# Optimization experiments

Measured on AMD Instinct MI355X. Metric: run time of the kernel, lower is better.

Reference implementation:

```python
import jax, jax.numpy as jnp
import numpy as np

N = 100000          # nodes
E = 1600000         # edges
F = 128             # input features
H = 128             # hidden_channels
G = 64              # graphs in batch


def setup_inputs() -> dict:
    key = jax.random.key(0)
    ks = jax.random.split(key, 16)
    x = jax.random.normal(ks[0], (N, F), dtype=jnp.float32)
    edge_index = jax.random.randint(ks[1], (2, E), 0, N, dtype=jnp.int32)
    batch = jnp.sort(jax.random.randint(ks[2], (N,), 0, G, dtype=jnp.int32))

    def glorot(k, fan_in, fan_out):
        s = jnp.sqrt(6.0 / (fan_in + fan_out)).astype(jnp.float32)
        return jax.random.uniform(k, (fan_in, fan_out), jnp.float32, -s, s)

    return {
        "x": x, "edge_index": edge_index, "batch": batch,
        "W1": glorot(ks[3], F, H),       "b1": jnp.zeros((H,), jnp.float32),
        "W2": glorot(ks[4], H, H),       "b2": jnp.zeros((H,), jnp.float32),
        "W3": glorot(ks[5], H, 2 * H),   "b3": jnp.zeros((2 * H,), jnp.float32),
        "W4": glorot(ks[6], 2 * H, H),   "b4": jnp.zeros((H,), jnp.float32),
        "Wl": glorot(ks[7], F, H),       "bl": jnp.zeros((H,), jnp.float32),
    }


def _gcn_conv(x, W, b, src, dst, deg_inv_sqrt):
    # PyG GCNConv: add self-loops, symmetric normalization D^-1/2 (A+I) D^-1/2
    h = x @ W                                  # [N, out]
    norm = deg_inv_sqrt[src] * deg_inv_sqrt[dst]      # [E]
    msg = h[src] * norm[:, None]               # gather + scale, [E, out]
    agg = jax.ops.segment_sum(msg, dst, num_segments=N)
    agg = agg + h * (deg_inv_sqrt * deg_inv_sqrt)[:, None]  # self-loop term (norm = 1/deg)
    return agg + b


def reference(x, edge_index, batch, W1, b1, W2, b2, W3, b3, W4, b4, Wl, bl):
    src, dst = edge_index[0], edge_index[1]
    # degree (incl. self-loop) from dst, as in PyG gcn_norm
    deg = jax.ops.segment_sum(jnp.ones((E,), jnp.float32), dst, num_segments=N) + 1.0
    deg_inv_sqrt = jax.lax.rsqrt(deg)

    identity = x
    x = jax.nn.relu(_gcn_conv(x, W1, b1, src, dst, deg_inv_sqrt))
    x = jax.nn.relu(_gcn_conv(x, W2, b2, src, dst, deg_inv_sqrt))
    x = jax.nn.relu(_gcn_conv(x, W3, b3, src, dst, deg_inv_sqrt))
    x = _gcn_conv(x, W4, b4, src, dst, deg_inv_sqrt)
    x = x + (identity @ Wl + bl)

    # global_mean_pool over graph ids
    sums = jax.ops.segment_sum(x, batch, num_segments=G)
    cnts = jax.ops.segment_sum(jnp.ones((N,), jnp.float32), batch, num_segments=G)
    return sums / jnp.maximum(cnts, 1.0)[:, None]
```

## Files before the change

kernel.cpp:

```cpp
#include <hip/hip_runtime.h>

#define NN 100000
#define EE 1600000
#define GG 64
#define PCHUNK 1024
#define PBLK 1563
#define NBUCK 196

typedef __attribute__((ext_vector_type(8))) short short8v;
typedef __attribute__((ext_vector_type(4))) float f32x4;

__device__ __forceinline__ unsigned short f2bf(float f) {
    unsigned u = __float_as_uint(f);
    u = (u + 0x7FFFu + ((u >> 16) & 1)) >> 16;
    return (unsigned short)u;
}
__device__ __forceinline__ float bf2f(unsigned short s) {
    return __uint_as_float((unsigned)s << 16);
}

__global__ __launch_bounds__(256) void partitionA_kernel(const int* __restrict__ src,
                                                         const int* __restrict__ dst,
                                                         int* __restrict__ cnt,
                                                         int* __restrict__ ghist,
                                                         int* __restrict__ gboff,
                                                         int2* __restrict__ stage) {
    __shared__ int hist[NBUCK];
    __shared__ int sc[256];
    __shared__ int boff[NBUCK];
    __shared__ int bcur[NBUCK];
    int b = blockIdx.x, t = threadIdx.x;
    int e0 = b * PCHUNK;
    int n = EE - e0;
    if (n > PCHUNK) n = PCHUNK;
    if (t < NBUCK) { hist[t] = 0; bcur[t] = 0; }
    __syncthreads();
    int dv[4], sv[4];
#pragma unroll
    for (int j = 0; j < 4; ++j) {
        int i = t + j * 256;
        if (i < n) {
            dv[j] = dst[e0 + i];
            sv[j] = src[e0 + i];
            atomicAdd(&cnt[dv[j]], 1);
            atomicAdd(&hist[dv[j] >> 9], 1);
        }
    }
    __syncthreads();
    sc[t] = (t < NBUCK) ? hist[t] : 0;
    __syncthreads();
    for (int off = 1; off < 256; off <<= 1) {
        int a = (t >= off) ? sc[t - off] : 0;
        __syncthreads();
        sc[t] += a;
        __syncthreads();
    }
    if (t < NBUCK) boff[t] = sc[t] - hist[t];
    __syncthreads();
#pragma unroll
    for (int j = 0; j < 4; ++j) {
        int i = t + j * 256;
        if (i < n) {
            int k = dv[j] >> 9;
            int p = boff[k] + atomicAdd(&bcur[k], 1);
            stage[(size_t)b * PCHUNK + p] = make_int2(sv[j], dv[j]);
        }
    }
    if (t < NBUCK) {
        ghist[b * NBUCK + t] = hist[t];
        gboff[b * NBUCK + t] = boff[t];
    }
}

__global__ __launch_bounds__(256) void dis_kernel(const int* __restrict__ cnt,
                                                  float* __restrict__ dis) {
    int i = blockIdx.x * 256 + threadIdx.x;
    if (i < NN) dis[i] = rsqrtf((float)cnt[i] + 1.0f);
}

#define SCAN_EPB 1024
__global__ __launch_bounds__(256) void scan_block_kernel(const int* __restrict__ in,
                                                         int* __restrict__ out,
                                                         int* __restrict__ bsums) {
    __shared__ int sd[256];
    int t = threadIdx.x;
    int base = blockIdx.x * SCAN_EPB + t * 4;
    int v[4];
#pragma unroll
    for (int j = 0; j < 4; ++j) v[j] = (base + j < NN) ? in[base + j] : 0;
    int s = v[0] + v[1] + v[2] + v[3];
    sd[t] = s;
    __syncthreads();
    for (int off = 1; off < 256; off <<= 1) {
        int add = (t >= off) ? sd[t - off] : 0;
        __syncthreads();
        sd[t] += add;
        __syncthreads();
    }
    int ex = sd[t] - s;
    int run = ex;
#pragma unroll
    for (int j = 0; j < 4; ++j) {
        if (base + j < NN) out[base + j] = run;
        run += v[j];
    }
    if (t == 255) bsums[blockIdx.x] = sd[255];
}

__global__ void scan_sums_kernel(int* __restrict__ bsums, int nb) {
    if (threadIdx.x == 0 && blockIdx.x == 0) {
        int run = 0;
        for (int i = 0; i < nb; ++i) {
            int v = bsums[i];
            bsums[i] = run;
            run += v;
        }
    }
}

__global__ __launch_bounds__(256) void scan_add_kernel(int* __restrict__ rs,
                                                       const int* __restrict__ bsums,
                                                       int* __restrict__ cursor) {
    int i = blockIdx.x * 256 + threadIdx.x;
    if (i < NN) {
        int v = rs[i] + bsums[i >> 10];
        rs[i] = v;
        cursor[i] = v;
    }
    if (i == 0) rs[NN] = EE;
}

__global__ __launch_bounds__(256) void scatterC_kernel(const int2* __restrict__ stage,
                                                       const int* __restrict__ ghist,
                                                       const int* __restrict__ gboff,
                                                       int* __restrict__ cursor,
                                                       int* __restrict__ csr) {
    int k = blockIdx.x;
    int b = blockIdx.y * 256 + threadIdx.x;
    if (b >= PBLK) return;
    int c_ = ghist[b * NBUCK + k];
    size_t base = (size_t)b * PCHUNK + gboff[b * NBUCK + k];
    for (int i = 0; i < c_; ++i) {
        int2 e = stage[base + i];
        int p = atomicAdd(&cursor[e.y], 1);
        csr[p] = e.x;
    }
}

__global__ __launch_bounds__(256) void cvt_kernel(const float* __restrict__ x,
                                                  const float* __restrict__ dis,
                                                  unsigned short* __restrict__ xb) {
    size_t i = ((size_t)blockIdx.x * 256 + threadIdx.x) * 8;
    float d = dis[i >> 7];
    float4 a = *(const float4*)(x + i);
    float4 b = *(const float4*)(x + i + 4);
    short8v v;
    v[0] = (short)f2bf(a.x * d); v[1] = (short)f2bf(a.y * d);
    v[2] = (short)f2bf(a.z * d); v[3] = (short)f2bf(a.w * d);
    v[4] = (short)f2bf(b.x * d); v[5] = (short)f2bf(b.y * d);
    v[6] = (short)f2bf(b.z * d); v[7] = (short)f2bf(b.w * d);
    *(short8v*)(xb + i) = v;
}

template <int K, int M>
__global__ __launch_bounds__(64) void packw_kernel(const float* __restrict__ W,
                                                   unsigned short* __restrict__ Wp) {
    const int NKS = K / 32;
    int ct = blockIdx.x / NKS, ks = blockIdx.x % NKS;
    int lane = threadIdx.x;
    int col = ct * 16 + (lane & 15);
    int kb = ks * 32 + (lane >> 4) * 8;
    unsigned short* o = Wp + ((size_t)(ct * NKS + ks) * 64 + lane) * 16;
#pragma unroll
    for (int i = 0; i < 8; ++i) {
        float f = W[(size_t)(kb + i) * M + col];
        unsigned short h = f2bf(f);
        unsigned short l = f2bf(f - bf2f(h));
        o[i] = h;
        o[8 + i] = l;
    }
}

template <int K, int M, int RT, bool ASPLIT, bool RELU, bool BIAS, bool ACCUM, bool DSCALE>
__global__ __launch_bounds__(256) void gemm_kernel(const void* __restrict__ Ain,
                                                   const unsigned short* __restrict__ Wp,
                                                   const float* __restrict__ bias,
                                                   const float* __restrict__ dis,
                                                   void* __restrict__ out) {
    const int NKS = K / 32;
    int tid = threadIdx.x;
    int wave = tid >> 6, lane = tid & 63;
    int r0 = blockIdx.x * (RT * 64) + wave * (RT * 16);

    short8v ah[RT][NKS];
    short8v al[ASPLIT ? RT : 1][ASPLIT ? NKS : 1];
#pragma unroll
    for (int t = 0; t < RT; ++t) {
        int ra = r0 + t * 16 + (lane & 15);
        if (ra > NN - 1) ra = NN - 1;
        if (ASPLIT) {
            const float* A = (const float*)Ain;
#pragma unroll
            for (int ks = 0; ks < NKS; ++ks) {
                const float* p = A + (size_t)ra * K + ks * 32 + (lane >> 4) * 8;
                float4 v0 = *(const float4*)p;
                float4 v1 = *(const float4*)(p + 4);
                float f[8] = {v0.x, v0.y, v0.z, v0.w, v1.x, v1.y, v1.z, v1.w};
#pragma unroll
                for (int i = 0; i < 8; ++i) {
                    unsigned short h = f2bf(f[i]);
                    ah[t][ks][i] = (short)h;
                    al[t][ks][i] = (short)f2bf(f[i] - bf2f(h));
                }
            }
        } else {
            const unsigned short* A = (const unsigned short*)Ain;
#pragma unroll
            for (int ks = 0; ks < NKS; ++ks)
                ah[t][ks] = *(const short8v*)(A + (size_t)ra * K + ks * 32 + (lane >> 4) * 8);
        }
    }

    float dsc[RT][4];
#pragma unroll
    for (int t = 0; t < RT; ++t)
#pragma unroll
        for (int i = 0; i < 4; ++i) {
            int row = r0 + t * 16 + (lane >> 4) * 4 + i;
            dsc[t][i] = (DSCALE && row < NN) ? dis[row] : 1.f;
        }

#pragma unroll
    for (int ct = 0; ct < 8; ++ct) {
        int ctg = blockIdx.y * 8 + ct;
        int col = ctg * 16 + (lane & 15);
        float bv = BIAS ? bias[col] : 0.f;
        f32x4 acc[RT];
#pragma unroll
        for (int t = 0; t < RT; ++t) {
            acc[t][0] = bv; acc[t][1] = bv; acc[t][2] = bv; acc[t][3] = bv;
        }
#pragma unroll
        for (int ks = 0; ks < NKS; ++ks) {
            const short8v* pW = (const short8v*)Wp + ((size_t)(ctg * NKS + ks) * 64 + lane) * 2;
            short8v bh = pW[0], blo = pW[1];
#pragma unroll
            for (int t = 0; t < RT; ++t) {
                acc[t] = __builtin_amdgcn_mfma_f32_16x16x32_bf16(ah[t][ks], bh, acc[t], 0, 0, 0);
                acc[t] = __builtin_amdgcn_mfma_f32_16x16x32_bf16(ah[t][ks], blo, acc[t], 0, 0, 0);
                if (ASPLIT)
                    acc[t] = __builtin_amdgcn_mfma_f32_16x16x32_bf16(al[t][ks], bh, acc[t], 0, 0, 0);
            }
        }
#pragma unroll
        for (int t = 0; t < RT; ++t)
#pragma unroll
            for (int i = 0; i < 4; ++i) {
                int row = r0 + t * 16 + (lane >> 4) * 4 + i;
                if (row >= NN) continue;
                float v = acc[t][i];
                if (RELU) v = fmaxf(v, 0.f);
                if (ACCUM) {
                    ((float*)out)[(size_t)row * M + col] += v;
                } else {
                    ((unsigned short*)out)[(size_t)row * M + col] = f2bf(v * dsc[t][i]);
                }
            }
    }
}

template <int OUTMODE>
__global__ __launch_bounds__(256) void aggb_kernel(const unsigned short* __restrict__ h,
                                                   const float* __restrict__ dis,
                                                   const int* __restrict__ csr,
                                                   const int* __restrict__ rs,
                                                   const float* __restrict__ bias,
                                                   void* __restrict__ out) {
    int node = blockIdx.x * 4 + (threadIdx.x >> 6);
    int lane = threadIdx.x & 63;
    if (node >= NN) return;
    int c = lane & 15;
    int s = lane >> 4;
    int beg = rs[node], end = rs[node + 1];
    const uint4* hb = (const uint4*)h;
    float acc[8] = {};
    for (int e0 = beg; e0 < end; e0 += 32) {
        int myidx = 0;
        int el = e0 + lane;
        if (lane < 32 && el < end) myidx = csr[el];
        uint4 v[8];
#pragma unroll
        for (int j = 0; j < 8; ++j) {
            int sidx = __shfl(myidx, j * 4 + s, 64);
            v[j] = make_uint4(0u, 0u, 0u, 0u);
            int ej = e0 + j * 4 + s;
            if (ej < end) v[j] = hb[(size_t)sidx * 16 + c];
        }
#pragma unroll
        for (int j = 0; j < 8; ++j) {
            acc[0] += __uint_as_float(v[j].x << 16);
            acc[1] += __uint_as_float(v[j].x & 0xFFFF0000u);
            acc[2] += __uint_as_float(v[j].y << 16);
            acc[3] += __uint_as_float(v[j].y & 0xFFFF0000u);
            acc[4] += __uint_as_float(v[j].z << 16);
            acc[5] += __uint_as_float(v[j].z & 0xFFFF0000u);
            acc[6] += __uint_as_float(v[j].w << 16);
            acc[7] += __uint_as_float(v[j].w & 0xFFFF0000u);
        }
    }
#pragma unroll
    for (int i = 0; i < 8; ++i) {
        acc[i] += __shfl_xor(acc[i], 16, 64);
        acc[i] += __shfl_xor(acc[i], 32, 64);
    }
    if (s == 0) {
        float d = dis[node];
        uint4 us = hb[(size_t)node * 16 + c];
        float sf[8];
        sf[0] = __uint_as_float(us.x << 16); sf[1] = __uint_as_float(us.x & 0xFFFF0000u);
        sf[2] = __uint_as_float(us.y << 16); sf[3] = __uint_as_float(us.y & 0xFFFF0000u);
        sf[4] = __uint_as_float(us.z << 16); sf[5] = __uint_as_float(us.z & 0xFFFF0000u);
        sf[6] = __uint_as_float(us.w << 16); sf[7] = __uint_as_float(us.w & 0xFFFF0000u);
        float r[8];
#pragma unroll
        for (int i = 0; i < 8; ++i) r[i] = d * (acc[i] + sf[i]);
        if (OUTMODE == 0) {
            uint4 o;
            o.x = (unsigned)f2bf(r[0]) | ((unsigned)f2bf(r[1]) << 16);
            o.y = (unsigned)f2bf(r[2]) | ((unsigned)f2bf(r[3]) << 16);
            o.z = (unsigned)f2bf(r[4]) | ((unsigned)f2bf(r[5]) << 16);
            o.w = (unsigned)f2bf(r[6]) | ((unsigned)f2bf(r[7]) << 16);
            ((uint4*)out)[(size_t)node * 16 + c] = o;
        } else {
#pragma unroll
            for (int i = 0; i < 8; ++i) r[i] += bias[c * 8 + i];
            float4 o0 = make_float4(r[0], r[1], r[2], r[3]);
            float4 o1 = make_float4(r[4], r[5], r[6], r[7]);
            float* O = (float*)out + (size_t)node * 128 + c * 8;
            *(float4*)O = o0;
            *(float4*)(O + 4) = o1;
        }
    }
}

__global__ __launch_bounds__(128) void pool_partial_kernel(const float* __restrict__ y,
                                                           const int* __restrict__ batch,
                                                           float* __restrict__ P) {
    int c = threadIdx.x;
    int chunk = (NN + gridDim.x - 1) / gridDim.x;
    int n0 = blockIdx.x * chunk;
    int n1 = n0 + chunk;
    if (n1 > NN) n1 = NN;
    if (n0 >= NN) return;
    int curg = batch[n0];
    float acc = 0.f;
    for (int n = n0; n < n1; ++n) {
        int g = batch[n];
        if (g != curg) {
            atomicAdd(&P[curg * 128 + c], acc);
            acc = 0.f;
            curg = g;
        }
        acc += y[(size_t)n * 128 + c];
    }
    atomicAdd(&P[curg * 128 + c], acc);
}

__global__ __launch_bounds__(128) void pool_final_kernel(const float* __restrict__ P,
                                                         const int* __restrict__ batch,
                                                         float* __restrict__ out) {
    int g = blockIdx.x, c = threadIdx.x;
    int lo = 0, hi = NN;
    while (lo < hi) {
        int m = (lo + hi) >> 1;
        if (batch[m] < g) lo = m + 1;
        else hi = m;
    }
    int start = lo;
    int lo2 = start, hi2 = NN;
    while (lo2 < hi2) {
        int m = (lo2 + hi2) >> 1;
        if (batch[m] < g + 1) lo2 = m + 1;
        else hi2 = m;
    }
    float cntg = (float)(lo2 - start);
    out[g * 128 + c] = P[g * 128 + c] / fmaxf(cntg, 1.f);
}

extern "C" void kernel_launch(void* const* d_in, const int* in_sizes, int n_in,
                              void* d_out, int out_size, void* d_ws, size_t ws_size,
                              hipStream_t stream) {
    const float* x = (const float*)d_in[0];
    const int* ei = (const int*)d_in[1];
    const int* batch = (const int*)d_in[2];
    const float* W1 = (const float*)d_in[3];
    const float* b1 = (const float*)d_in[4];
    const float* W2 = (const float*)d_in[5];
    const float* b2 = (const float*)d_in[6];
    const float* W3 = (const float*)d_in[7];
    const float* b3 = (const float*)d_in[8];
    const float* W4 = (const float*)d_in[9];
    const float* b4 = (const float*)d_in[10];
    const float* Wl = (const float*)d_in[11];
    const float* bl = (const float*)d_in[12];
    float* out = (float*)d_out;

    char* p = (char*)d_ws;
    auto alloc = [&](size_t bytes) {
        void* r = (void*)p;
        p += (bytes + 255) & ~(size_t)255;
        return r;
    };
    int* cnt = (int*)alloc((size_t)NN * 4);
    int* rs = (int*)alloc((size_t)(NN + 1) * 4);
    int* cursor = (int*)alloc((size_t)NN * 4);
    float* dis = (float*)alloc((size_t)NN * 4);
    const int NB = (NN + SCAN_EPB - 1) / SCAN_EPB;
    int* bsums = (int*)alloc((size_t)NB * 4);
    int* csr = (int*)alloc((size_t)EE * 4);
    int* ghist = (int*)alloc((size_t)PBLK * NBUCK * 4);
    int* gboff = (int*)alloc((size_t)PBLK * NBUCK * 4);
    unsigned short* xb = (unsigned short*)alloc((size_t)NN * 128 * 2);
    unsigned short* AG = (unsigned short*)alloc((size_t)NN * 128 * 2);
    unsigned short* GM = (unsigned short*)alloc((size_t)NN * 128 * 2);
    unsigned short* H3 = (unsigned short*)alloc((size_t)NN * 256 * 2);
    float* Y = (float*)alloc((size_t)NN * 128 * 4);
    unsigned short* W1p = (unsigned short*)alloc(8 * 4 * 64 * 16 * 2);
    unsigned short* W2p = (unsigned short*)alloc(8 * 4 * 64 * 16 * 2);
    unsigned short* W3p = (unsigned short*)alloc(16 * 4 * 64 * 16 * 2);
    unsigned short* W4p = (unsigned short*)alloc(8 * 8 * 64 * 16 * 2);
    unsigned short* Wlp = (unsigned short*)alloc(8 * 4 * 64 * 16 * 2);
    float* P = (float*)alloc((size_t)GG * 128 * 4);
    int2* stage = (int2*)Y;

    const int* src = ei;
    const int* dst = ei + EE;

    hipMemsetAsync(cnt, 0, (size_t)NN * 4, stream);
    hipMemsetAsync(P, 0, (size_t)GG * 128 * 4, stream);

    partitionA_kernel<<<PBLK, 256, 0, stream>>>(src, dst, cnt, ghist, gboff, stage);
    dis_kernel<<<(NN + 255) / 256, 256, 0, stream>>>(cnt, dis);
    cvt_kernel<<<(NN * 128) / (256 * 8), 256, 0, stream>>>(x, dis, xb);
    scan_block_kernel<<<NB, 256, 0, stream>>>(cnt, rs, bsums);
    scan_sums_kernel<<<1, 64, 0, stream>>>(bsums, NB);
    scan_add_kernel<<<(NN + 255) / 256, 256, 0, stream>>>(rs, bsums, cursor);
    scatterC_kernel<<<dim3(NBUCK, (PBLK + 255) / 256), 256, 0, stream>>>(stage, ghist, gboff, cursor, csr);

    packw_kernel<128, 128><<<8 * 4, 64, 0, stream>>>(W1, W1p);
    packw_kernel<128, 128><<<8 * 4, 64, 0, stream>>>(W2, W2p);
    packw_kernel<128, 256><<<16 * 4, 64, 0, stream>>>(W3, W3p);
    packw_kernel<256, 128><<<8 * 8, 64, 0, stream>>>(W4, W4p);
    packw_kernel<128, 128><<<8 * 4, 64, 0, stream>>>(Wl, Wlp);

    const int AGG_GRID = (NN + 3) / 4;
    const int GX4 = (NN + 255) / 256;
    const int GX2 = (NN + 127) / 128;

    aggb_kernel<0><<<AGG_GRID, 256, 0, stream>>>(xb, dis, csr, rs, nullptr, AG);
    gemm_kernel<128, 128, 4, false, true, true, false, true><<<dim3(GX4, 1), 256, 0, stream>>>(AG, W1p, b1, dis, GM);
    aggb_kernel<0><<<AGG_GRID, 256, 0, stream>>>(GM, dis, csr, rs, nullptr, AG);
    gemm_kernel<128, 128, 4, false, true, true, false, true><<<dim3(GX4, 1), 256, 0, stream>>>(AG, W2p, b2, dis, GM);
    aggb_kernel<0><<<AGG_GRID, 256, 0, stream>>>(GM, dis, csr, rs, nullptr, AG);
    gemm_kernel<128, 256, 4, false, true, true, false, false><<<dim3(GX4, 2), 256, 0, stream>>>(AG, W3p, b3, nullptr, H3);
    gemm_kernel<256, 128, 2, false, false, false, false, true><<<dim3(GX2, 1), 256, 0, stream>>>(H3, W4p, nullptr, dis, AG);
    aggb_kernel<1><<<AGG_GRID, 256, 0, stream>>>(AG, dis, csr, rs, b4, Y);
    gemm_kernel<128, 128, 2, true, false, true, true, false><<<dim3(GX2, 1), 256, 0, stream>>>(x, Wlp, bl, nullptr, Y);
    pool_partial_kernel<<<512, 128, 0, stream>>>(Y, batch, P);
    pool_final_kernel<<<GG, 128, 0, stream>>>(P, batch, out);
}
```

Baseline: 798.4 us.

## Replace multi-pass CSR build with two-pass bucket sort and per-bucket local CSR

Rebuilds the CSR construction as a two-level bucket sort. A first kernel atomically reserves slots per 512-node bucket in fixed-capacity staging regions. A single-block scan then computes bucket bases, and a per-bucket kernel builds node histograms, row starts, degree normalisation and CSR entries entirely in shared memory. This drops the global per-node count atomics, the multi-kernel scan and the scatter kernel that used global cursor atomics. The trade-off is a fixed per-bucket capacity (BWCAP) that silently drops edges if a bucket overflows, which only holds for evenly spread destinations. CSR order within a node also becomes nondeterministic.

```diff
diff --git a/kernel.cpp b/kernel.cpp
--- a/kernel.cpp
+++ b/kernel.cpp
@@ -3,9 +3,10 @@
 #define NN 100000
 #define EE 1600000
 #define GG 64
-#define PCHUNK 1024
-#define PBLK 1563
+#define PCHUNK 2048
+#define PBLK1 782
 #define NBUCK 196
+#define BWCAP 12288
 
 typedef __attribute__((ext_vector_type(8))) short short8v;
 typedef __attribute__((ext_vector_type(4))) float f32x4;
@@ -19,35 +20,50 @@
     return __uint_as_float((unsigned)s << 16);
 }
 
-__global__ __launch_bounds__(256) void partitionA_kernel(const int* __restrict__ src,
-                                                         const int* __restrict__ dst,
-                                                         int* __restrict__ cnt,
-                                                         int* __restrict__ ghist,
-                                                         int* __restrict__ gboff,
-                                                         int2* __restrict__ stage) {
+__global__ __launch_bounds__(256) void bucketK1_kernel(const int* __restrict__ src,
+                                                       const int* __restrict__ dst,
+                                                       int* __restrict__ gcur,
+                                                       int2* __restrict__ stage) {
     __shared__ int hist[NBUCK];
-    __shared__ int sc[256];
-    __shared__ int boff[NBUCK];
-    __shared__ int bcur[NBUCK];
+    __shared__ int base[NBUCK];
+    __shared__ int cur[NBUCK];
     int b = blockIdx.x, t = threadIdx.x;
     int e0 = b * PCHUNK;
     int n = EE - e0;
     if (n > PCHUNK) n = PCHUNK;
-    if (t < NBUCK) { hist[t] = 0; bcur[t] = 0; }
-    __syncthreads();
-    int dv[4], sv[4];
-#pragma unroll
-    for (int j = 0; j < 4; ++j) {
+    if (t < NBUCK) { hist[t] = 0; cur[t] = 0; }
+    __syncthreads();
+    int dv[8], sv[8];
+#pragma unroll
+    for (int j = 0; j < 8; ++j) {
         int i = t + j * 256;
         if (i < n) {
             dv[j] = dst[e0 + i];
             sv[j] = src[e0 + i];
-            atomicAdd(&cnt[dv[j]], 1);
             atomicAdd(&hist[dv[j] >> 9], 1);
         }
     }
     __syncthreads();
-    sc[t] = (t < NBUCK) ? hist[t] : 0;
+    if (t < NBUCK && hist[t] > 0) base[t] = atomicAdd(&gcur[t], hist[t]);
+    __syncthreads();
+#pragma unroll
+    for (int j = 0; j < 8; ++j) {
+        int i = t + j * 256;
+        if (i < n) {
+            int k = dv[j] >> 9;
+            int p = base[k] + atomicAdd(&cur[k], 1);
+            if (p < BWCAP) stage[(size_t)k * BWCAP + p] = make_int2(sv[j], dv[j]);
+        }
+    }
+}
+
+__global__ __launch_bounds__(256) void kscan_kernel(const int* __restrict__ gcur,
+                                                    int* __restrict__ bbase,
+                                                    int* __restrict__ rs) {
+    __shared__ int sc[256];
+    int t = threadIdx.x;
+    int v = (t < NBUCK) ? gcur[t] : 0;
+    sc[t] = v;
     __syncthreads();
     for (int off = 1; off < 256; off <<= 1) {
         int a = (t >= off) ? sc[t - off] : 0;
@@ -55,95 +71,58 @@
         sc[t] += a;
         __syncthreads();
     }
-    if (t < NBUCK) boff[t] = sc[t] - hist[t];
-    __syncthreads();
-#pragma unroll
-    for (int j = 0; j < 4; ++j) {
-        int i = t + j * 256;
-        if (i < n) {
-            int k = dv[j] >> 9;
-            int p = boff[k] + atomicAdd(&bcur[k], 1);
-            stage[(size_t)b * PCHUNK + p] = make_int2(sv[j], dv[j]);
-        }
-    }
-    if (t < NBUCK) {
-        ghist[b * NBUCK + t] = hist[t];
-        gboff[b * NBUCK + t] = boff[t];
-    }
-}
-
-__global__ __launch_bounds__(256) void dis_kernel(const int* __restrict__ cnt,
-                                                  float* __restrict__ dis) {
-    int i = blockIdx.x * 256 + threadIdx.x;
-    if (i < NN) dis[i] = rsqrtf((float)cnt[i] + 1.0f);
-}
-
-#define SCAN_EPB 1024
-__global__ __launch_bounds__(256) void scan_block_kernel(const int* __restrict__ in,
-                                                         int* __restrict__ out,
-                                                         int* __restrict__ bsums) {
-    __shared__ int sd[256];
-    int t = threadIdx.x;
-    int base = blockIdx.x * SCAN_EPB + t * 4;
-    int v[4];
-#pragma unroll
-    for (int j = 0; j < 4; ++j) v[j] = (base + j < NN) ? in[base + j] : 0;
-    int s = v[0] + v[1] + v[2] + v[3];
-    sd[t] = s;
+    if (t < NBUCK) bbase[t] = sc[t] - v;
+    if (t == 0) rs[NN] = EE;
+}
+
+__global__ __launch_bounds__(256) void buildK2_kernel(const int2* __restrict__ stage,
+                                                      const int* __restrict__ gcur,
+                                                      const int* __restrict__ bbase,
+                                                      float* __restrict__ dis,
+                                                      int* __restrict__ rs,
+                                                      int* __restrict__ csr) {
+    __shared__ int hist[512];
+    __shared__ int lrs[512];
+    __shared__ int cur[512];
+    __shared__ int sc[256];
+    int k = blockIdx.x, t = threadIdx.x;
+    int cnt_ = gcur[k];
+    if (cnt_ > BWCAP) cnt_ = BWCAP;
+    const int2* W = stage + (size_t)k * BWCAP;
+    hist[t] = 0; hist[t + 256] = 0;
+    cur[t] = 0; cur[t + 256] = 0;
+    __syncthreads();
+    for (int i = t; i < cnt_; i += 256) atomicAdd(&hist[W[i].y & 511], 1);
+    __syncthreads();
+    int h0 = hist[2 * t], h1 = hist[2 * t + 1];
+    sc[t] = h0 + h1;
     __syncthreads();
     for (int off = 1; off < 256; off <<= 1) {
-        int add = (t >= off) ? sd[t - off] : 0;
+        int a = (t >= off) ? sc[t - off] : 0;
         __syncthreads();
-        sd[t] += add;
+        sc[t] += a;
         __syncthreads();
     }
-    int ex = sd[t] - s;
-    int run = ex;
-#pragma unroll
-    for (int j = 0; j < 4; ++j) {
-        if (base + j < NN) out[base + j] = run;
-        run += v[j];
-    }
-    if (t == 255) bsums[blockIdx.x] = sd[255];
-}
-
-__global__ void scan_sums_kernel(int* __restrict__ bsums, int nb) {
-    if (threadIdx.x == 0 && blockIdx.x == 0) {
-        int run = 0;
-        for (int i = 0; i < nb; ++i) {
-            int v = bsums[i];
-            bsums[i] = run;
-            run += v;
-        }
-    }
-}
-
-__global__ __launch_bounds__(256) void scan_add_kernel(int* __restrict__ rs,
-                                                       const int* __restrict__ bsums,
-                                                       int* __restrict__ cursor) {
-    int i = blockIdx.x * 256 + threadIdx.x;
-    if (i < NN) {
-        int v = rs[i] + bsums[i >> 10];
-        rs[i] = v;
-        cursor[i] = v;
-    }
-    if (i == 0) rs[NN] = EE;
-}
-
-__global__ __launch_bounds__(256) void scatterC_kernel(const int2* __restrict__ stage,
-                                                       const int* __restrict__ ghist,
-                                                       const int* __restrict__ gboff,
-                                                       int* __restrict__ cursor,
-                                                       int* __restrict__ csr) {
-    int k = blockIdx.x;
-    int b = blockIdx.y * 256 + threadIdx.x;
-    if (b >= PBLK) return;
-    int c_ = ghist[b * NBUCK + k];
-    size_t base = (size_t)b * PCHUNK + gboff[b * NBUCK + k];
-    for (int i = 0; i < c_; ++i) {
-        int2 e = stage[base + i];
-        int p = atomicAdd(&cursor[e.y], 1);
-        csr[p] = e.x;
+    int ex = sc[t] - (h0 + h1);
+    lrs[2 * t] = ex;
+    lrs[2 * t + 1] = ex + h0;
+    __syncthreads();
+    int bb = bbase[k];
+#pragma unroll
+    for (int q = 0; q < 2; ++q) {
+        int nl = t + q * 256;
+        int node = k * 512 + nl;
+        if (node < NN) {
+            rs[node] = bb + lrs[nl];
+            dis[node] = rsqrtf((float)hist[nl] + 1.0f);
+        }
+    }
+    __syncthreads();
+    for (int i = t; i < cnt_; i += 256) {
+        int2 e = W[i];
+        int nl = e.y & 511;
+        int p = lrs[nl] + atomicAdd(&cur[nl], 1);
+        csr[bb + p] = e.x;
     }
 }
 
@@ -411,15 +390,11 @@
         p += (bytes + 255) & ~(size_t)255;
         return r;
     };
-    int* cnt = (int*)alloc((size_t)NN * 4);
     int* rs = (int*)alloc((size_t)(NN + 1) * 4);
-    int* cursor = (int*)alloc((size_t)NN * 4);
     float* dis = (float*)alloc((size_t)NN * 4);
-    const int NB = (NN + SCAN_EPB - 1) / SCAN_EPB;
-    int* bsums = (int*)alloc((size_t)NB * 4);
+    int* gcur = (int*)alloc((size_t)NBUCK * 4);
+    int* bbase = (int*)alloc((size_t)(NBUCK + 4) * 4);
     int* csr = (int*)alloc((size_t)EE * 4);
-    int* ghist = (int*)alloc((size_t)PBLK * NBUCK * 4);
-    int* gboff = (int*)alloc((size_t)PBLK * NBUCK * 4);
     unsigned short* xb = (unsigned short*)alloc((size_t)NN * 128 * 2);
     unsigned short* AG = (unsigned short*)alloc((size_t)NN * 128 * 2);
     unsigned short* GM = (unsigned short*)alloc((size_t)NN * 128 * 2);
@@ -436,17 +411,14 @@
     const int* src = ei;
     const int* dst = ei + EE;
 
-    hipMemsetAsync(cnt, 0, (size_t)NN * 4, stream);
+    hipMemsetAsync(gcur, 0, (size_t)NBUCK * 4, stream);
     hipMemsetAsync(P, 0, (size_t)GG * 128 * 4, stream);
 
-    partitionA_kernel<<<PBLK, 256, 0, stream>>>(src, dst, cnt, ghist, gboff, stage);
-    dis_kernel<<<(NN + 255) / 256, 256, 0, stream>>>(cnt, dis);
+    bucketK1_kernel<<<PBLK1, 256, 0, stream>>>(src, dst, gcur, stage);
+    kscan_kernel<<<1, 256, 0, stream>>>(gcur, bbase, rs);
+    buildK2_kernel<<<NBUCK, 256, 0, stream>>>(stage, gcur, bbase, dis, rs, csr);
+
     cvt_kernel<<<(NN * 128) / (256 * 8), 256, 0, stream>>>(x, dis, xb);
-    scan_block_kernel<<<NB, 256, 0, stream>>>(cnt, rs, bsums);
-    scan_sums_kernel<<<1, 64, 0, stream>>>(bsums, NB);
-    scan_add_kernel<<<(NN + 255) / 256, 256, 0, stream>>>(rs, bsums, cursor);
-    scatterC_kernel<<<dim3(NBUCK, (PBLK + 255) / 256), 256, 0, stream>>>(stage, ghist, gboff, cursor, csr);
-
     packw_kernel<128, 128><<<8 * 4, 64, 0, stream>>>(W1, W1p);
     packw_kernel<128, 128><<<8 * 4, 64, 0, stream>>>(W2, W2p);
     packw_kernel<128, 256><<<16 * 4, 64, 0, stream>>>(W3, W3p);
```

Result: faster. 694.0 us (-13.1%).
